# Performance work log

Hardware: AMD Instinct MI355X
Metric: run time of the kernel (lower is better)

Reference implementation:

```python
import jax, jax.numpy as jnp
import numpy as np

B, N_UNITS, IN_FEATURES = 8192, 512, 64
TOPK = 8


def setup_inputs() -> dict:
    key = jax.random.key(0)
    kx, kc = jax.random.split(key)
    x = jax.random.normal(kx, (B, IN_FEATURES), dtype=jnp.float32)
    # centroid param: truncated_normal(stddev=1.0) per flax initializer
    c = jax.random.truncated_normal(kc, -2.0, 2.0, (N_UNITS, IN_FEATURES)).astype(jnp.float32)
    return {"x": x, "c": c, "topk": TOPK}


def reference(x, c, topk):
    # pairwise Euclidean distances: [B, n_units]
    d = jnp.sqrt(((x[..., None, :] - c) ** 2).sum(-1))
    # i_sort[b, j] = index of j-th closest centroid
    i_sort = jnp.argsort(d, axis=-1)
    # k[b, u] = rank of centroid u (argsort of argsort)
    k = jnp.argsort(i_sort, axis=-1)
    # top-k scatter: z[b, i_sort[b, j]] = 1/(j+1) for j < topk
    idx_topk = i_sort[..., :topk]                       # [B, topk]
    vals = 1.0 / jnp.arange(1.0, topk + 1, dtype=jnp.float32)  # [topk]
    rows = jnp.arange(d.shape[0])[:, None]              # [B, 1]
    z = jnp.zeros(d.shape, dtype=jnp.float32).at[rows, idx_topk].set(vals)
    # nearest-centroid gather
    x_c = c[i_sort[..., 0]]                             # [B, in_features]
    return (d, i_sort, k, z, x_c)
```

## Files before the change

kernel.cpp:

```cpp
#include <hip/hip_runtime.h>
#include <math.h>

#define B_ROWS 8192
#define NU 512
#define FEATS 64
#define RPB 8
#define TOPK_K 8

typedef unsigned long long ull;

__device__ __forceinline__ ull shfl_xor_u64(ull x, int m) {
  int lo = (int)(unsigned)(x & 0xffffffffULL);
  int hi = (int)(unsigned)(x >> 32);
  lo = __shfl_xor(lo, m, 64);
  hi = __shfl_xor(hi, m, 64);
  return ((ull)(unsigned)hi << 32) | (ull)(unsigned)lo;
}

template <int S>
__device__ __forceinline__ void inreg_pass(ull v[8], unsigned lane, unsigned k) {
#pragma unroll
  for (int i = 0; i < 8; ++i) {
    if ((i & S) == 0) {
      const int ip = i | S;
      const unsigned e = (lane << 3) | (unsigned)i;
      const bool asc = ((e & k) == 0);
      const ull a = v[i], b = v[ip];
      const bool lt = a < b;
      const ull lo2 = lt ? a : b;
      const ull hi2 = lt ? b : a;
      v[i]  = asc ? lo2 : hi2;
      v[ip] = asc ? hi2 : lo2;
    }
  }
}

__device__ __forceinline__ void cross_pass(ull v[8], unsigned lane, unsigned m, unsigned k) {
#pragma unroll
  for (int i = 0; i < 8; ++i) {
    const ull o = shfl_xor_u64(v[i], (int)m);
    const unsigned e = (lane << 3) | (unsigned)i;
    const bool takeMin = (((lane & m) == 0) == ((e & k) == 0));
    const bool keep = ((v[i] < o) == takeMin);
    v[i] = keep ? v[i] : o;
  }
}

__global__ __launch_bounds__(512, 2)
void lcm_kernel(const float* __restrict__ x, const float* __restrict__ c,
                float* __restrict__ out) {
#pragma clang fp contract(off)
  __shared__ ull keys[RPB * NU];

  const int t = threadIdx.x;
  const int r0 = blockIdx.x * RPB;

  {
    const int n = t;
    float4 cs4[16];
    const float4* c4 = (const float4*)c + (size_t)n * 16;
#pragma unroll
    for (int q = 0; q < 16; ++q) cs4[q] = c4[q];
#pragma unroll
    for (int q = 0; q < 16; ++q) {
      asm volatile("" : "+v"(cs4[q].x), "+v"(cs4[q].y),
                        "+v"(cs4[q].z), "+v"(cs4[q].w));
    }

    float* o_d = out;
#pragma unroll
    for (int r = 0; r < RPB; ++r) {
      const float* __restrict__ xr = x + (size_t)(r0 + r) * FEATS;
      float rr[16];
#pragma unroll
      for (int k = 0; k < 4; ++k) {
        const float4 xq0 = *(const float4*)(xr + 16 * k + 0);
        const float4 xq1 = *(const float4*)(xr + 16 * k + 4);
        const float4 xq2 = *(const float4*)(xr + 16 * k + 8);
        const float4 xq3 = *(const float4*)(xr + 16 * k + 12);
        const float4 xq[4] = {xq0, xq1, xq2, xq3};
#pragma unroll
        for (int q = 0; q < 4; ++q) {
          const float4 cv = cs4[k * 4 + q];
          const float4 xv = xq[q];
          const float t0 = xv.x - cv.x;
          const float t1 = xv.y - cv.y;
          const float t2 = xv.z - cv.z;
          const float t3 = xv.w - cv.w;
          if (k == 0) {
            rr[q * 4 + 0] = t0 * t0;
            rr[q * 4 + 1] = t1 * t1;
            rr[q * 4 + 2] = t2 * t2;
            rr[q * 4 + 3] = t3 * t3;
          } else {
            rr[q * 4 + 0] = rr[q * 4 + 0] + t0 * t0;
            rr[q * 4 + 1] = rr[q * 4 + 1] + t1 * t1;
            rr[q * 4 + 2] = rr[q * 4 + 2] + t2 * t2;
            rr[q * 4 + 3] = rr[q * 4 + 3] + t3 * t3;
          }
        }
      }
      float s8[8], s4[4], s2[2];
#pragma unroll
      for (int j = 0; j < 8; ++j) s8[j] = rr[j] + rr[j + 8];
#pragma unroll
      for (int j = 0; j < 4; ++j) s4[j] = s8[j] + s8[j + 4];
#pragma unroll
      for (int j = 0; j < 2; ++j) s2[j] = s4[j] + s4[j + 2];
      const float tot = s2[0] + s2[1];
      const float dv = (float)__builtin_sqrt((double)tot);
      o_d[(size_t)(r0 + r) * NU + n] = dv;
      keys[r * NU + n] = ((ull)__float_as_uint(dv) << 32) | (ull)n;
    }
  }
  __syncthreads();

  {
    const unsigned lane = (unsigned)(t & 63);
    const int w = t >> 6;

    ull v[8];
#pragma unroll
    for (int i = 0; i < 8; ++i) v[i] = keys[w * NU + i * 64 + (int)lane];

    inreg_pass<1>(v, lane, 2u);
    inreg_pass<2>(v, lane, 4u);
    inreg_pass<1>(v, lane, 4u);
    inreg_pass<4>(v, lane, 8u);
    inreg_pass<2>(v, lane, 8u);
    inreg_pass<1>(v, lane, 8u);
    for (unsigned k = 16; k <= 512; k <<= 1) {
      for (unsigned j = k >> 1; j >= 8; j >>= 1) cross_pass(v, lane, j >> 3, k);
      inreg_pass<4>(v, lane, k);
      inreg_pass<2>(v, lane, k);
      inreg_pass<1>(v, lane, k);
    }

    const int row = r0 + w;
    float* o_is = out + (size_t)B_ROWS * NU;
    float* o_k  = o_is + (size_t)B_ROWS * NU;
    float* o_z  = o_k + (size_t)B_ROWS * NU;
    float* o_xc = o_z + (size_t)B_ROWS * NU;

    int idxv[8];
#pragma unroll
    for (int i = 0; i < 8; ++i) idxv[i] = (int)(v[i] & 0x1ffULL);

    float4 fa, fb;
    fa.x = (float)idxv[0]; fa.y = (float)idxv[1];
    fa.z = (float)idxv[2]; fa.w = (float)idxv[3];
    fb.x = (float)idxv[4]; fb.y = (float)idxv[5];
    fb.z = (float)idxv[6]; fb.w = (float)idxv[7];
    float4* isrow = (float4*)(o_is + (size_t)row * NU);
    isrow[lane * 2 + 0] = fa;
    isrow[lane * 2 + 1] = fb;

#pragma unroll
    for (int i = 0; i < 8; ++i) {
      const int e = (int)lane * 8 + i;
      o_k[(size_t)row * NU + idxv[i]] = (float)e;
      o_z[(size_t)row * NU + idxv[i]] = (e < TOPK_K) ? (1.0f / (float)(i + 1)) : 0.0f;
    }

    int top = idxv[0];
    top = __shfl(top, 0, 64);
    o_xc[(size_t)row * FEATS + (int)lane] = c[top * FEATS + (int)lane];
  }
}

extern "C" void kernel_launch(void* const* d_in, const int* in_sizes, int n_in,
                              void* d_out, int out_size, void* d_ws, size_t ws_size,
                              hipStream_t stream) {
  const float* x = (const float*)d_in[0];
  const float* c = (const float*)d_in[1];
  float* out = (float*)d_out;
  lcm_kernel<<<dim3(B_ROWS / RPB), dim3(512), 0, stream>>>(x, c, out);
}
```

Before: 131.1 us.

## Use DPP and bpermute shuffles with compile-time bitonic stages

Rewrites the per-wave bitonic sort so each stage is a template with compile-time direction masks. Cross-lane exchanges at distance 1 and 2 now use DPP quad permutes, and longer distances use ds_bpermute with precomputed addresses instead of __shfl_xor. The aim is to cut shuffle latency and the per-element direction arithmetic during the sort. It also drops the min-2-waves occupancy hint and the asm register pinning of centroids, which could change register allocation and occupancy.

Measured after the change: 128.5 us. 2.0% less time.

```diff
diff --git a/kernel.cpp b/kernel.cpp
--- a/kernel.cpp
+++ b/kernel.cpp
@@ -9,44 +9,63 @@
 
 typedef unsigned long long ull;
 
-__device__ __forceinline__ ull shfl_xor_u64(ull x, int m) {
+template <int CTRL>
+__device__ __forceinline__ ull dpp_u64(ull x) {
   int lo = (int)(unsigned)(x & 0xffffffffULL);
   int hi = (int)(unsigned)(x >> 32);
-  lo = __shfl_xor(lo, m, 64);
-  hi = __shfl_xor(hi, m, 64);
+  lo = __builtin_amdgcn_update_dpp(lo, lo, CTRL, 0xf, 0xf, true);
+  hi = __builtin_amdgcn_update_dpp(hi, hi, CTRL, 0xf, 0xf, true);
   return ((ull)(unsigned)hi << 32) | (ull)(unsigned)lo;
 }
 
-template <int S>
-__device__ __forceinline__ void inreg_pass(ull v[8], unsigned lane, unsigned k) {
+__device__ __forceinline__ ull bperm_u64(int addr, ull x) {
+  int lo = (int)(unsigned)(x & 0xffffffffULL);
+  int hi = (int)(unsigned)(x >> 32);
+  lo = __builtin_amdgcn_ds_bpermute(addr, lo);
+  hi = __builtin_amdgcn_ds_bpermute(addr, hi);
+  return ((ull)(unsigned)hi << 32) | (ull)(unsigned)lo;
+}
+
+__device__ __forceinline__ void ce(ull& a, ull& b, bool asc) {
+  const bool lt = a < b;
+  const bool sw = (lt != asc);
+  const ull t = sw ? b : a;
+  b = sw ? a : b;
+  a = t;
+}
+
+template <unsigned M, unsigned KB>
+__device__ __forceinline__ void cross_t(ull v[8], unsigned lane, int addr) {
+  const bool asc = ((lane & KB) == 0u);
+  const bool takeMin = (((lane & M) == 0u) == asc);
 #pragma unroll
   for (int i = 0; i < 8; ++i) {
-    if ((i & S) == 0) {
-      const int ip = i | S;
-      const unsigned e = (lane << 3) | (unsigned)i;
-      const bool asc = ((e & k) == 0);
-      const ull a = v[i], b = v[ip];
-      const bool lt = a < b;
-      const ull lo2 = lt ? a : b;
-      const ull hi2 = lt ? b : a;
-      v[i]  = asc ? lo2 : hi2;
-      v[ip] = asc ? hi2 : lo2;
-    }
-  }
-}
-
-__device__ __forceinline__ void cross_pass(ull v[8], unsigned lane, unsigned m, unsigned k) {
-#pragma unroll
-  for (int i = 0; i < 8; ++i) {
-    const ull o = shfl_xor_u64(v[i], (int)m);
-    const unsigned e = (lane << 3) | (unsigned)i;
-    const bool takeMin = (((lane & m) == 0) == ((e & k) == 0));
+    ull o;
+    if constexpr (M == 1)      o = dpp_u64<0xB1>(v[i]);
+    else if constexpr (M == 2) o = dpp_u64<0x4E>(v[i]);
+    else                       o = bperm_u64(addr, v[i]);
     const bool keep = ((v[i] < o) == takeMin);
     v[i] = keep ? v[i] : o;
   }
 }
 
-__global__ __launch_bounds__(512, 2)
+template <unsigned K>
+__device__ __forceinline__ void stage_t(ull v[8], unsigned lane,
+                                        int a4, int a8, int a16, int a32) {
+  constexpr unsigned KB = (K >> 3);
+  if constexpr (K >= 512) cross_t<32, KB>(v, lane, a32);
+  if constexpr (K >= 256) cross_t<16, KB>(v, lane, a16);
+  if constexpr (K >= 128) cross_t<8,  KB>(v, lane, a8);
+  if constexpr (K >= 64)  cross_t<4,  KB>(v, lane, a4);
+  if constexpr (K >= 32)  cross_t<2,  KB>(v, lane, 0);
+  cross_t<1, KB>(v, lane, 0);
+  const bool asc = ((lane & KB) == 0u);
+  ce(v[0], v[4], asc); ce(v[1], v[5], asc); ce(v[2], v[6], asc); ce(v[3], v[7], asc);
+  ce(v[0], v[2], asc); ce(v[1], v[3], asc); ce(v[4], v[6], asc); ce(v[5], v[7], asc);
+  ce(v[0], v[1], asc); ce(v[2], v[3], asc); ce(v[4], v[5], asc); ce(v[6], v[7], asc);
+}
+
+__global__ __launch_bounds__(512)
 void lcm_kernel(const float* __restrict__ x, const float* __restrict__ c,
                 float* __restrict__ out) {
 #pragma clang fp contract(off)
@@ -61,11 +80,6 @@
     const float4* c4 = (const float4*)c + (size_t)n * 16;
 #pragma unroll
     for (int q = 0; q < 16; ++q) cs4[q] = c4[q];
-#pragma unroll
-    for (int q = 0; q < 16; ++q) {
-      asm volatile("" : "+v"(cs4[q].x), "+v"(cs4[q].y),
-                        "+v"(cs4[q].z), "+v"(cs4[q].w));
-    }
 
     float* o_d = out;
 #pragma unroll
@@ -123,18 +137,29 @@
 #pragma unroll
     for (int i = 0; i < 8; ++i) v[i] = keys[w * NU + i * 64 + (int)lane];
 
-    inreg_pass<1>(v, lane, 2u);
-    inreg_pass<2>(v, lane, 4u);
-    inreg_pass<1>(v, lane, 4u);
-    inreg_pass<4>(v, lane, 8u);
-    inreg_pass<2>(v, lane, 8u);
-    inreg_pass<1>(v, lane, 8u);
-    for (unsigned k = 16; k <= 512; k <<= 1) {
-      for (unsigned j = k >> 1; j >= 8; j >>= 1) cross_pass(v, lane, j >> 3, k);
-      inreg_pass<4>(v, lane, k);
-      inreg_pass<2>(v, lane, k);
-      inreg_pass<1>(v, lane, k);
+    ce(v[0], v[1], true);  ce(v[2], v[3], false);
+    ce(v[4], v[5], true);  ce(v[6], v[7], false);
+    ce(v[0], v[2], true);  ce(v[1], v[3], true);
+    ce(v[4], v[6], false); ce(v[5], v[7], false);
+    ce(v[0], v[1], true);  ce(v[2], v[3], true);
+    ce(v[4], v[5], false); ce(v[6], v[7], false);
+    {
+      const bool a8 = ((lane & 1u) == 0u);
+      ce(v[0], v[4], a8); ce(v[1], v[5], a8); ce(v[2], v[6], a8); ce(v[3], v[7], a8);
+      ce(v[0], v[2], a8); ce(v[1], v[3], a8); ce(v[4], v[6], a8); ce(v[5], v[7], a8);
+      ce(v[0], v[1], a8); ce(v[2], v[3], a8); ce(v[4], v[5], a8); ce(v[6], v[7], a8);
     }
+
+    const int ad4  = (int)((lane ^ 4u)  << 2);
+    const int ad8  = (int)((lane ^ 8u)  << 2);
+    const int ad16 = (int)((lane ^ 16u) << 2);
+    const int ad32 = (int)((lane ^ 32u) << 2);
+    stage_t<16>(v, lane, ad4, ad8, ad16, ad32);
+    stage_t<32>(v, lane, ad4, ad8, ad16, ad32);
+    stage_t<64>(v, lane, ad4, ad8, ad16, ad32);
+    stage_t<128>(v, lane, ad4, ad8, ad16, ad32);
+    stage_t<256>(v, lane, ad4, ad8, ad16, ad32);
+    stage_t<512>(v, lane, ad4, ad8, ad16, ad32);
 
     const int row = r0 + w;
     float* o_is = out + (size_t)B_ROWS * NU;
```

## Sort 32-bit quantized keys with DPP shuffles and add exact-tie fallback kernel

Applied to the files above, without the earlier changes.

Packs each distance into a 32-bit key: the float bits are offset from 4.0, clamped and shifted into 23 bits, with the 9-bit index in the low bits. This replaces the 64-bit keys, halving shuffle and compare work in the bitonic sort. Short-distance lane exchanges use DPP and longer ones use ds_bpermute. The rank (k) and z outputs are built by inverting the permutation in LDS and writing coalesced float4 rows instead of scattered global stores. Rows with possible ties after quantization are flagged, and a second kernel redoes those rows exactly with 64-bit keys. This adds an extra launch plus the risk that many rows get flagged.

Result: faster. 128.5 us (-2.0%).

```diff
diff --git a/kernel.cpp b/kernel.cpp
--- a/kernel.cpp
+++ b/kernel.cpp
@@ -8,6 +8,48 @@
 #define TOPK_K 8
 
 typedef unsigned long long ull;
+
+__device__ __forceinline__ void ce32(unsigned& a, unsigned& b, bool asc) {
+  const unsigned mn = a < b ? a : b;
+  const unsigned mx = a < b ? b : a;
+  a = asc ? mn : mx;
+  b = asc ? mx : mn;
+}
+
+template <unsigned M, unsigned KB>
+__device__ __forceinline__ void cross32(unsigned v[8], unsigned lane, int addr) {
+  const bool asc = ((lane & KB) == 0u);
+  const bool takeMin = (((lane & M) == 0u) == asc);
+#pragma unroll
+  for (int i = 0; i < 8; ++i) {
+    unsigned o;
+    if constexpr (M == 1)
+      o = (unsigned)__builtin_amdgcn_update_dpp((int)v[i], (int)v[i], 0xB1, 0xf, 0xf, true);
+    else if constexpr (M == 2)
+      o = (unsigned)__builtin_amdgcn_update_dpp((int)v[i], (int)v[i], 0x4E, 0xf, 0xf, true);
+    else
+      o = (unsigned)__builtin_amdgcn_ds_bpermute(addr, (int)v[i]);
+    const unsigned mn = v[i] < o ? v[i] : o;
+    const unsigned mx = v[i] < o ? o : v[i];
+    v[i] = takeMin ? mn : mx;
+  }
+}
+
+template <unsigned K>
+__device__ __forceinline__ void stage32(unsigned v[8], unsigned lane,
+                                        int a4, int a8, int a16, int a32) {
+  constexpr unsigned KB = (K >> 3);
+  if constexpr (K >= 512) cross32<32, KB>(v, lane, a32);
+  if constexpr (K >= 256) cross32<16, KB>(v, lane, a16);
+  if constexpr (K >= 128) cross32<8,  KB>(v, lane, a8);
+  if constexpr (K >= 64)  cross32<4,  KB>(v, lane, a4);
+  if constexpr (K >= 32)  cross32<2,  KB>(v, lane, 0);
+  cross32<1, KB>(v, lane, 0);
+  const bool asc = ((lane & KB) == 0u);
+  ce32(v[0], v[4], asc); ce32(v[1], v[5], asc); ce32(v[2], v[6], asc); ce32(v[3], v[7], asc);
+  ce32(v[0], v[2], asc); ce32(v[1], v[3], asc); ce32(v[4], v[6], asc); ce32(v[5], v[7], asc);
+  ce32(v[0], v[1], asc); ce32(v[2], v[3], asc); ce32(v[4], v[5], asc); ce32(v[6], v[7], asc);
+}
 
 __device__ __forceinline__ ull shfl_xor_u64(ull x, int m) {
   int lo = (int)(unsigned)(x & 0xffffffffULL);
@@ -46,14 +88,17 @@
   }
 }
 
-__global__ __launch_bounds__(512, 2)
+__global__ __launch_bounds__(512)
 void lcm_kernel(const float* __restrict__ x, const float* __restrict__ c,
-                float* __restrict__ out) {
+                float* __restrict__ out, unsigned* __restrict__ flags) {
 #pragma clang fp contract(off)
-  __shared__ ull keys[RPB * NU];
+  __shared__ unsigned keys[RPB * NU];
+  __shared__ float ztab[9];
 
   const int t = threadIdx.x;
   const int r0 = blockIdx.x * RPB;
+
+  if (t < 9) ztab[t] = (t < 8) ? (1.0f / (float)(t + 1)) : 0.0f;
 
   {
     const int n = t;
@@ -61,11 +106,6 @@
     const float4* c4 = (const float4*)c + (size_t)n * 16;
 #pragma unroll
     for (int q = 0; q < 16; ++q) cs4[q] = c4[q];
-#pragma unroll
-    for (int q = 0; q < 16; ++q) {
-      asm volatile("" : "+v"(cs4[q].x), "+v"(cs4[q].y),
-                        "+v"(cs4[q].z), "+v"(cs4[q].w));
-    }
 
     float* o_d = out;
 #pragma unroll
@@ -88,10 +128,8 @@
           const float t2 = xv.z - cv.z;
           const float t3 = xv.w - cv.w;
           if (k == 0) {
-            rr[q * 4 + 0] = t0 * t0;
-            rr[q * 4 + 1] = t1 * t1;
-            rr[q * 4 + 2] = t2 * t2;
-            rr[q * 4 + 3] = t3 * t3;
+            rr[q * 4 + 0] = t0 * t0; rr[q * 4 + 1] = t1 * t1;
+            rr[q * 4 + 2] = t2 * t2; rr[q * 4 + 3] = t3 * t3;
           } else {
             rr[q * 4 + 0] = rr[q * 4 + 0] + t0 * t0;
             rr[q * 4 + 1] = rr[q * 4 + 1] + t1 * t1;
@@ -110,7 +148,16 @@
       const float tot = s2[0] + s2[1];
       const float dv = (float)__builtin_sqrt((double)tot);
       o_d[(size_t)(r0 + r) * NU + n] = dv;
-      keys[r * NU + n] = ((ull)__float_as_uint(dv) << 32) | (ull)n;
+
+      const unsigned db = __float_as_uint(dv);
+      unsigned q;
+      if (db < 0x40800000u) q = 0u;
+      else {
+        const unsigned off = db - 0x40800000u;
+        q = off > 0x00FFFFFFu ? 0x00FFFFFFu : off;
+      }
+      q >>= 1;
+      keys[r * NU + n] = (q << 9) | (unsigned)n;
     }
   }
   __syncthreads();
@@ -119,22 +166,32 @@
     const unsigned lane = (unsigned)(t & 63);
     const int w = t >> 6;
 
-    ull v[8];
+    unsigned v[8];
 #pragma unroll
     for (int i = 0; i < 8; ++i) v[i] = keys[w * NU + i * 64 + (int)lane];
 
-    inreg_pass<1>(v, lane, 2u);
-    inreg_pass<2>(v, lane, 4u);
-    inreg_pass<1>(v, lane, 4u);
-    inreg_pass<4>(v, lane, 8u);
-    inreg_pass<2>(v, lane, 8u);
-    inreg_pass<1>(v, lane, 8u);
-    for (unsigned k = 16; k <= 512; k <<= 1) {
-      for (unsigned j = k >> 1; j >= 8; j >>= 1) cross_pass(v, lane, j >> 3, k);
-      inreg_pass<4>(v, lane, k);
-      inreg_pass<2>(v, lane, k);
-      inreg_pass<1>(v, lane, k);
+    ce32(v[0], v[1], true);  ce32(v[2], v[3], false);
+    ce32(v[4], v[5], true);  ce32(v[6], v[7], false);
+    ce32(v[0], v[2], true);  ce32(v[1], v[3], true);
+    ce32(v[4], v[6], false); ce32(v[5], v[7], false);
+    ce32(v[0], v[1], true);  ce32(v[2], v[3], true);
+    ce32(v[4], v[5], false); ce32(v[6], v[7], false);
+    {
+      const bool a8 = ((lane & 1u) == 0u);
+      ce32(v[0], v[4], a8); ce32(v[1], v[5], a8); ce32(v[2], v[6], a8); ce32(v[3], v[7], a8);
+      ce32(v[0], v[2], a8); ce32(v[1], v[3], a8); ce32(v[4], v[6], a8); ce32(v[5], v[7], a8);
+      ce32(v[0], v[1], a8); ce32(v[2], v[3], a8); ce32(v[4], v[5], a8); ce32(v[6], v[7], a8);
     }
+    const int ad4  = (int)((lane ^ 4u)  << 2);
+    const int ad8  = (int)((lane ^ 8u)  << 2);
+    const int ad16 = (int)((lane ^ 16u) << 2);
+    const int ad32 = (int)((lane ^ 32u) << 2);
+    stage32<16>(v, lane, ad4, ad8, ad16, ad32);
+    stage32<32>(v, lane, ad4, ad8, ad16, ad32);
+    stage32<64>(v, lane, ad4, ad8, ad16, ad32);
+    stage32<128>(v, lane, ad4, ad8, ad16, ad32);
+    stage32<256>(v, lane, ad4, ad8, ad16, ad32);
+    stage32<512>(v, lane, ad4, ad8, ad16, ad32);
 
     const int row = r0 + w;
     float* o_is = out + (size_t)B_ROWS * NU;
@@ -144,7 +201,7 @@
 
     int idxv[8];
 #pragma unroll
-    for (int i = 0; i < 8; ++i) idxv[i] = (int)(v[i] & 0x1ffULL);
+    for (int i = 0; i < 8; ++i) idxv[i] = (int)(v[i] & 0x1ffu);
 
     float4 fa, fb;
     fa.x = (float)idxv[0]; fa.y = (float)idxv[1];
@@ -155,17 +212,101 @@
     isrow[lane * 2 + 0] = fa;
     isrow[lane * 2 + 1] = fb;
 
-#pragma unroll
-    for (int i = 0; i < 8; ++i) {
-      const int e = (int)lane * 8 + i;
-      o_k[(size_t)row * NU + idxv[i]] = (float)e;
-      o_z[(size_t)row * NU + idxv[i]] = (e < TOPK_K) ? (1.0f / (float)(i + 1)) : 0.0f;
-    }
+    unsigned* krow = keys + w * NU;
+#pragma unroll
+    for (int i = 0; i < 8; ++i) krow[idxv[i]] = (unsigned)(lane * 8 + i);
+    asm volatile("s_waitcnt lgkmcnt(0)" ::: "memory");
+    const uint4 ka = ((const uint4*)krow)[lane * 2 + 0];
+    const uint4 kb = ((const uint4*)krow)[lane * 2 + 1];
+
+    float4 k0, k1;
+    k0.x = (float)ka.x; k0.y = (float)ka.y; k0.z = (float)ka.z; k0.w = (float)ka.w;
+    k1.x = (float)kb.x; k1.y = (float)kb.y; k1.z = (float)kb.z; k1.w = (float)kb.w;
+    float4* krow_g = (float4*)(o_k + (size_t)row * NU);
+    krow_g[lane * 2 + 0] = k0;
+    krow_g[lane * 2 + 1] = k1;
+
+    float4 z0, z1;
+    z0.x = ztab[ka.x < 8u ? ka.x : 8u]; z0.y = ztab[ka.y < 8u ? ka.y : 8u];
+    z0.z = ztab[ka.z < 8u ? ka.z : 8u]; z0.w = ztab[ka.w < 8u ? ka.w : 8u];
+    z1.x = ztab[kb.x < 8u ? kb.x : 8u]; z1.y = ztab[kb.y < 8u ? kb.y : 8u];
+    z1.z = ztab[kb.z < 8u ? kb.z : 8u]; z1.w = ztab[kb.w < 8u ? kb.w : 8u];
+    float4* zrow_g = (float4*)(o_z + (size_t)row * NU);
+    zrow_g[lane * 2 + 0] = z0;
+    zrow_g[lane * 2 + 1] = z1;
 
     int top = idxv[0];
     top = __shfl(top, 0, 64);
     o_xc[(size_t)row * FEATS + (int)lane] = c[top * FEATS + (int)lane];
-  }
+
+    bool tie = false;
+#pragma unroll
+    for (int i = 0; i < 7; ++i) tie |= ((v[i] >> 9) == (v[i + 1] >> 9));
+    const unsigned q0 = v[0] >> 9;
+    const unsigned q7 = v[7] >> 9;
+    const unsigned nq0 = (unsigned)__shfl_down((int)q0, 1, 64);
+    if (lane < 63) tie |= (q7 == nq0);
+    const ull tb = __ballot(tie);
+    if (lane == 0) flags[row] = (tb != 0ULL) ? 1u : 0u;
+  }
+}
+
+__global__ __launch_bounds__(64)
+void fix_kernel(const float* __restrict__ c, float* __restrict__ out,
+                const unsigned* __restrict__ flags) {
+  const int row = blockIdx.x;
+  if (flags[row] == 0u) return;
+  const unsigned lane = threadIdx.x;
+
+  const float* drow = out + (size_t)row * NU;
+  ull v[8];
+#pragma unroll
+  for (int i = 0; i < 8; ++i) {
+    const float dv = drow[i * 64 + (int)lane];
+    v[i] = ((ull)__float_as_uint(dv) << 32) | (ull)(unsigned)(i * 64 + (int)lane);
+  }
+
+  inreg_pass<1>(v, lane, 2u);
+  inreg_pass<2>(v, lane, 4u);
+  inreg_pass<1>(v, lane, 4u);
+  inreg_pass<4>(v, lane, 8u);
+  inreg_pass<2>(v, lane, 8u);
+  inreg_pass<1>(v, lane, 8u);
+  for (unsigned k = 16; k <= 512; k <<= 1) {
+    for (unsigned j = k >> 1; j >= 8; j >>= 1) cross_pass(v, lane, j >> 3, k);
+    inreg_pass<4>(v, lane, k);
+    inreg_pass<2>(v, lane, k);
+    inreg_pass<1>(v, lane, k);
+  }
+
+  float* o_is = out + (size_t)B_ROWS * NU;
+  float* o_k  = o_is + (size_t)B_ROWS * NU;
+  float* o_z  = o_k + (size_t)B_ROWS * NU;
+  float* o_xc = o_z + (size_t)B_ROWS * NU;
+
+  int idxv[8];
+#pragma unroll
+  for (int i = 0; i < 8; ++i) idxv[i] = (int)(v[i] & 0x1ffULL);
+
+  float4 fa, fb;
+  fa.x = (float)idxv[0]; fa.y = (float)idxv[1];
+  fa.z = (float)idxv[2]; fa.w = (float)idxv[3];
+  fb.x = (float)idxv[4]; fb.y = (float)idxv[5];
+  fb.z = (float)idxv[6]; fb.w = (float)idxv[7];
+  float4* isrow = (float4*)(o_is + (size_t)row * NU);
+  isrow[lane * 2 + 0] = fa;
+  isrow[lane * 2 + 1] = fb;
+
+#pragma unroll
+  for (int i = 0; i < 8; ++i) {
+    const int e = (int)lane * 8 + i;
+    o_k[(size_t)row * NU + idxv[i]] = (float)e;
+    o_z[(size_t)row * NU + idxv[i]] = (e < TOPK_K) ? (1.0f / (float)(i + 1)) : 0.0f;
+  }
+
+  int top = idxv[0];
+  top = __shfl(top, 0, 64);
+  o_xc[(size_t)row * FEATS + (int)lane] = c[top * FEATS + (int)lane];
 }
 
 extern "C" void kernel_launch(void* const* d_in, const int* in_sizes, int n_in,
@@ -174,5 +315,7 @@
   const float* x = (const float*)d_in[0];
   const float* c = (const float*)d_in[1];
   float* out = (float*)d_out;
-  lcm_kernel<<<dim3(B_ROWS / RPB), dim3(512), 0, stream>>>(x, c, out);
-}
+  unsigned* flags = (unsigned*)d_ws;
+  lcm_kernel<<<dim3(B_ROWS / RPB), dim3(512), 0, stream>>>(x, c, out, flags);
+  fix_kernel<<<dim3(B_ROWS), dim3(64), 0, stream>>>(c, out, flags);
+}
```
